# Kernel tuning notes

Measured on AMD Instinct MI355X. Metric: run time of the kernel, lower is better.

The kernel has to match this reference:

```python
import jax, jax.numpy as jnp
import numpy as np

N_HEAD = 8

def setup_inputs() -> dict:
    key = jax.random.key(0)
    ks = jax.random.split(key, 5)
    B, T, C = 2, 4096, 512
    x = jax.random.normal(ks[0], (B, T, C), dtype=jnp.float32)
    w_attn = jax.random.normal(ks[1], (3 * C, C), dtype=jnp.float32) * (1.0 / np.sqrt(C))
    b_attn = jax.random.normal(ks[2], (3 * C,), dtype=jnp.float32) * 0.02
    w_proj = jax.random.normal(ks[3], (C, C), dtype=jnp.float32) * (1.0 / np.sqrt(C))
    b_proj = jax.random.normal(ks[4], (C,), dtype=jnp.float32) * 0.02
    return {"x": x, "w_attn": w_attn, "b_attn": b_attn, "w_proj": w_proj, "b_proj": b_proj}

def reference(x, w_attn, b_attn, w_proj, b_proj):
    B, T, C = x.shape
    H = N_HEAD
    D = C // H  # head dim
    qkv = x @ w_attn.T + b_attn  # [B,T,3C]
    q, k, v = jnp.split(qkv, 3, axis=-1)
    # b t (h d) -> b h t d
    def to_heads(t):
        return t.reshape(B, T, H, D).transpose(0, 2, 1, 3)
    q, k, v = to_heads(q), to_heads(k), to_heads(v)
    scale = 1.0 / np.sqrt(D).astype(np.float32)
    att = jnp.einsum('bhqd,bhkd->bhqk', q, k) * scale  # [B,H,T,T]
    causal = jnp.tril(jnp.ones((T, T), dtype=bool))
    att = jnp.where(causal[None, None], att, jnp.float32(-jnp.inf))
    att = jax.nn.softmax(att, axis=-1)
    y = jnp.einsum('bhqk,bhkd->bhqd', att, v)  # [B,H,T,D]
    y = y.transpose(0, 2, 1, 3).reshape(B, T, C)
    return y @ w_proj.T + b_proj
```

## Files before the change

### kernel.cpp

```cpp
#include <hip/hip_runtime.h>

typedef __attribute__((ext_vector_type(8))) __bf16 bf16x8;
typedef __attribute__((ext_vector_type(4))) __bf16 bf16x4;
typedef __attribute__((ext_vector_type(4))) float f32x4;
typedef __attribute__((ext_vector_type(16))) float f32x16;
typedef __attribute__((ext_vector_type(4))) unsigned uint32x4;
typedef __attribute__((ext_vector_type(2))) unsigned uint32x2;

#define AS1 __attribute__((address_space(1)))
#define AS3 __attribute__((address_space(3)))

#if __has_builtin(__builtin_amdgcn_exp2f)
#define EXP2(x) __builtin_amdgcn_exp2f(x)
#else
#define EXP2(x) exp2f(x)
#endif

#define QSCALE 0.18033688011112042f

#define N_X 4194304
#define N_WA 786432
#define N_WP 262144
__global__ __launch_bounds__(256) void convert_all_k(const float* __restrict__ x,
                                                     const float* __restrict__ wa,
                                                     const float* __restrict__ wp,
                                                     __bf16* __restrict__ xb,
                                                     __bf16* __restrict__ wab,
                                                     __bf16* __restrict__ wpb) {
  int i = (blockIdx.x * 256 + threadIdx.x) * 8;
  const float* src;
  __bf16* dst;
  int off;
  if (i < N_X)              { src = x;  dst = xb;  off = i; }
  else if (i < N_X + N_WA)  { src = wa; dst = wab; off = i - N_X; }
  else if (i < N_X + N_WA + N_WP) { src = wp; dst = wpb; off = i - N_X - N_WA; }
  else return;
  float4 v0 = *reinterpret_cast<const float4*>(src + off);
  float4 v1 = *reinterpret_cast<const float4*>(src + off + 4);
  bf16x8 o;
  o[0] = (__bf16)v0.x; o[1] = (__bf16)v0.y; o[2] = (__bf16)v0.z; o[3] = (__bf16)v0.w;
  o[4] = (__bf16)v1.x; o[5] = (__bf16)v1.y; o[6] = (__bf16)v1.z; o[7] = (__bf16)v1.w;
  *reinterpret_cast<bf16x8*>(dst + off) = o;
}

__global__ __launch_bounds__(256) void gemm_bt(const __bf16* __restrict__ A,
                                               const __bf16* __restrict__ Bm,
                                               const float* __restrict__ bias,
                                               void* __restrict__ outp,
                                               __bf16* __restrict__ vtout,
                                               int M, int N, int K) {
  __shared__ __bf16 smem[24576];
  const int tid = threadIdx.x;
  const int lane = tid & 63;
  const int w = tid >> 6;
  const int wm = w >> 1, wn = w & 1;
  const int ll = lane & 15, lh = lane >> 4;
  const int bid = (int)blockIdx.x;
  const int NT = N >> 7;
  const int xcd = bid & 7, lidx = bid >> 3;
  const int m0 = (xcd * 8 + lidx / NT) * 128;
  const int n0 = (lidx % NT) * 128;
  f32x4 acc[4][4] = {};

  auto stage = [&](int k0, int ss) {
    __bf16* al = smem + ss * 8192;
    __bf16* bl = al + 4096;
#pragma unroll
    for (int i = 0; i < 2; ++i) {
      int ch = i * 256 + tid;
      int r = ch >> 2, cs = (ch & 3) ^ ((r >> 1) & 3);
      const __bf16* ga = A + (size_t)(m0 + r) * K + k0 + cs * 8;
      __builtin_amdgcn_global_load_lds((const AS1 void*)ga, (AS3 void*)(al + ch * 8), 16, 0, 0);
      const __bf16* gb = Bm + (size_t)(n0 + r) * K + k0 + cs * 8;
      __builtin_amdgcn_global_load_lds((const AS1 void*)gb, (AS3 void*)(bl + ch * 8), 16, 0, 0);
    }
  };

  const int nsteps = K >> 5;
  stage(0, 0);
  __builtin_amdgcn_sched_barrier(0);
  stage(32, 1);
  __builtin_amdgcn_sched_barrier(0);
  int slot = 0;
  for (int t = 0; t < nsteps; ++t) {
    if (t + 1 < nsteps) asm volatile("s_waitcnt vmcnt(4)" ::: "memory");
    else                asm volatile("s_waitcnt vmcnt(0)" ::: "memory");
    __builtin_amdgcn_sched_barrier(0);
    __builtin_amdgcn_s_barrier();
    __builtin_amdgcn_sched_barrier(0);
    if (t + 2 < nsteps) {
      int s2 = slot + 2; if (s2 >= 3) s2 -= 3;
      stage((t + 2) << 5, s2);
      __builtin_amdgcn_sched_barrier(0);
    }
    const __bf16* al = smem + slot * 8192;
    const __bf16* bl = al + 4096;
    bf16x8 af[4], bfr[4];
#pragma unroll
    for (int m = 0; m < 4; ++m) {
      int R = wm * 64 + m * 16 + ll;
      af[m] = *reinterpret_cast<const bf16x8*>(al + R * 32 + ((lh ^ ((R >> 1) & 3)) << 3));
    }
#pragma unroll
    for (int n = 0; n < 4; ++n) {
      int R = wn * 64 + n * 16 + ll;
      bfr[n] = *reinterpret_cast<const bf16x8*>(bl + R * 32 + ((lh ^ ((R >> 1) & 3)) << 3));
    }
    __builtin_amdgcn_s_setprio(1);
#pragma unroll
    for (int m = 0; m < 4; ++m)
#pragma unroll
      for (int n = 0; n < 4; ++n)
        acc[m][n] = __builtin_amdgcn_mfma_f32_16x16x32_bf16(af[m], bfr[n], acc[m][n], 0, 0, 0);
    __builtin_amdgcn_s_setprio(0);
    __builtin_amdgcn_sched_barrier(0);
    slot = (slot == 2) ? 0 : slot + 1;
  }
  if (n0 < 1024) {
    __syncthreads();
    __bf16* tb = smem + w * 4096;
    const float sc = (n0 < 512) ? (float)QSCALE : 1.0f;
#pragma unroll
    for (int m = 0; m < 4; ++m)
#pragma unroll
      for (int n = 0; n < 4; ++n) {
        float bs = bias[n0 + wn * 64 + n * 16 + ll];
#pragma unroll
        for (int r = 0; r < 4; ++r)
          tb[(m * 16 + lh * 4 + r) * 64 + n * 16 + ll] = (__bf16)((acc[m][n][r] + bs) * sc);
      }
    const int rsub = lane >> 3, csub = (lane & 7) * 8;
#pragma unroll
    for (int i = 0; i < 8; ++i) {
      bf16x8 vv = *reinterpret_cast<const bf16x8*>(tb + (i * 8 + rsub) * 64 + csub);
      *reinterpret_cast<bf16x8*>((__bf16*)outp +
          (size_t)(m0 + wm * 64 + i * 8 + rsub) * N + n0 + wn * 64 + csub) = vv;
    }
  } else {
    __syncthreads();
    __bf16* tb = smem + w * 4096;
#pragma unroll
    for (int m = 0; m < 4; ++m) {
      const int rb = m * 4 + lh;
#pragma unroll
      for (int n = 0; n < 4; ++n) {
        const int col = n * 16 + ll;
        float bs = bias[n0 + wn * 64 + col];
        bf16x4 pk;
#pragma unroll
        for (int r = 0; r < 4; ++r) pk[r] = (__bf16)(acc[m][n][r] + bs);
        *reinterpret_cast<bf16x4*>(tb + col * 64 + ((rb ^ (col & 15)) << 2)) = pk;
      }
    }
    const int b = m0 >> 12;
    const int tbase = (m0 + wm * 64) & 4095;
    const int dbase = n0 - 1024 + wn * 64;
    const int dl = lane >> 3;
    const int j1 = (lane & 7) * 2;
    const int tloc = (lane & 7) * 8;
#pragma unroll
    for (int i = 0; i < 8; ++i) {
      const int col = i * 8 + dl;
      uint32x2 lo = *reinterpret_cast<const uint32x2*>(tb + col * 64 + ((j1 ^ (col & 15)) << 2));
      uint32x2 hi = *reinterpret_cast<const uint32x2*>(tb + col * 64 + (((j1 + 1) ^ (col & 15)) << 2));
      uint32x4 full = {lo[0], lo[1], hi[0], hi[1]};
      *reinterpret_cast<uint32x4*>(vtout + ((size_t)(b * 512 + dbase + col)) * 4096 + tbase + tloc) = full;
    }
  }
}

__global__ __launch_bounds__(256) void gemm2_k(const __bf16* __restrict__ A,
                                               const __bf16* __restrict__ Bm,
                                               const float* __restrict__ bias,
                                               float* __restrict__ out) {
  __shared__ __bf16 smem[12288];
  const int K = 512, N = 512;
  const int tid = threadIdx.x, lane = tid & 63, w = tid >> 6;
  const int wm = w >> 1, wn = w & 1;
  const int ll = lane & 15, lh = lane >> 4;
  const int bid = (int)blockIdx.x;
  const int xcd = bid & 7, lidx = bid >> 3;
  const int m0 = (xcd * 16 + (lidx >> 3)) * 64;
  const int n0 = (lidx & 7) * 64;
  f32x4 acc[2][2] = {};

  const int r = tid >> 2, cs = (tid & 3) ^ ((r >> 1) & 3);
  const __bf16* ga = A + (size_t)(m0 + r) * K + cs * 8;
  const __bf16* gb = Bm + (size_t)(n0 + r) * K + cs * 8;

  auto stage = [&](int k0, int ss) {
    __bf16* al = smem + ss * 4096;
    __builtin_amdgcn_global_load_lds((const AS1 void*)(ga + k0), (AS3 void*)(al + tid * 8), 16, 0, 0);
    __builtin_amdgcn_global_load_lds((const AS1 void*)(gb + k0), (AS3 void*)(al + 2048 + tid * 8), 16, 0, 0);
  };

  stage(0, 0);
  __builtin_amdgcn_sched_barrier(0);
  stage(32, 1);
  __builtin_amdgcn_sched_barrier(0);
  int slot = 0;
  for (int t = 0; t < 16; ++t) {
    if (t + 1 < 16) asm volatile("s_waitcnt vmcnt(2)" ::: "memory");
    else            asm volatile("s_waitcnt vmcnt(0)" ::: "memory");
    __builtin_amdgcn_sched_barrier(0);
    __builtin_amdgcn_s_barrier();
    __builtin_amdgcn_sched_barrier(0);
    if (t + 2 < 16) {
      int s2 = slot + 2; if (s2 >= 3) s2 -= 3;
      stage((t + 2) << 5, s2);
      __builtin_amdgcn_sched_barrier(0);
    }
    const __bf16* al = smem + slot * 4096;
    const __bf16* bl = al + 2048;
    bf16x8 af[2], bfr[2];
#pragma unroll
    for (int m = 0; m < 2; ++m) {
      int R = wm * 32 + m * 16 + ll;
      af[m] = *reinterpret_cast<const bf16x8*>(al + R * 32 + ((lh ^ ((R >> 1) & 3)) << 3));
    }
#pragma unroll
    for (int n = 0; n < 2; ++n) {
      int R = wn * 32 + n * 16 + ll;
      bfr[n] = *reinterpret_cast<const bf16x8*>(bl + R * 32 + ((lh ^ ((R >> 1) & 3)) << 3));
    }
    __builtin_amdgcn_s_setprio(1);
#pragma unroll
    for (int m = 0; m < 2; ++m)
#pragma unroll
      for (int n = 0; n < 2; ++n)
        acc[m][n] = __builtin_amdgcn_mfma_f32_16x16x32_bf16(af[m], bfr[n], acc[m][n], 0, 0, 0);
    __builtin_amdgcn_s_setprio(0);
    __builtin_amdgcn_sched_barrier(0);
    slot = (slot == 2) ? 0 : slot + 1;
  }
#pragma unroll
  for (int m = 0; m < 2; ++m) {
    int gm = m0 + wm * 32 + m * 16 + lh * 4;
#pragma unroll
    for (int n = 0; n < 2; ++n) {
      int gn = n0 + wn * 32 + n * 16 + ll;
      float bs = bias[gn];
#pragma unroll
      for (int r4 = 0; r4 < 4; ++r4)
        out[(size_t)(gm + r4) * N + gn] = acc[m][n][r4] + bs;
    }
  }
}

struct Tbl { unsigned short t[204]; };
constexpr Tbl build_tbl() {
  Tbl T{};
  int sizes[204] = {};
  int n = 0;
  for (int p = 0; p < 2; ++p)
    for (int qx = 0; qx < 32; ++qx) {
      int total = 2 * qx + 2;
      int nch = (total + 11) / 12;
      int cum = 0;
      for (int q = 0; q < qx; ++q) cum += (2 * q + 13) / 12;
      for (int c = 0; c < nch; ++c) {
        int sz = total - 12 * c; if (sz > 12) sz = 12;
        T.t[n] = (unsigned short)(qx | (c << 5) | (p << 8) | ((cum + c) << 9));
        sizes[n] = sz;
        ++n;
      }
    }
  for (int i = 1; i < n; ++i) {
    unsigned short tv = T.t[i]; int sv = sizes[i];
    int j = i - 1;
    while (j >= 0 && sizes[j] < sv) { T.t[j + 1] = T.t[j]; sizes[j + 1] = sizes[j]; --j; }
    T.t[j + 1] = tv; sizes[j + 1] = sv;
  }
  return T;
}
__device__ __constant__ Tbl g_tbl = build_tbl();

__device__ inline unsigned cvtpk(float lo, float hi_) {
  unsigned r;
  asm("v_cvt_pk_bf16_f32 %0, %1, %2" : "=v"(r) : "v"(lo), "v"(hi_));
  return r;
}

__global__ __launch_bounds__(256, 4) void attn_k(const __bf16* __restrict__ qkv,
                                                 const __bf16* __restrict__ vt,
                                                 __bf16* __restrict__ opart,
                                                 float* __restrict__ lpart,
                                                 __bf16* __restrict__ y) {
  __shared__ __bf16 k_lds[3][64 * 64];
  __shared__ __bf16 v_lds[2][64 * 64];
  const int tid = threadIdx.x, lane = tid & 63, w = tid >> 6;
  const int hi = lane >> 5, q31 = lane & 31;
  const int swz = q31 & 7;

  const int bid = (int)blockIdx.x;
  const int e = g_tbl.t[bid >> 3];
  const int qx = e & 31, c = (e >> 5) & 7, p = (e >> 8) & 1, j = e >> 9;
  const int bh = (bid & 7) * 2 + p;
  const int pslot = bh * 102 + j;
  const int b = bh >> 3, h = bh & 7;
  const int q0 = qx * 128;
  const int qw0 = q0 + w * 32;
  const int t0 = 12 * c;
  const int t1 = min(12 * c + 12, 2 * qx + 2);

  const __bf16* qp = qkv + (size_t)b * 4096 * 1536 + h * 64;
  const __bf16* vtp = vt + (size_t)(b * 512 + h * 64) * 4096;

  const int rr = tid >> 3;
  const int cs = (tid & 7) ^ (rr & 7);
  const __bf16* kg = qp + 512 + (size_t)(t0 * 64 + rr) * 1536 + cs * 8;
  const __bf16* vg = vtp + (size_t)rr * 4096 + t0 * 64 + cs * 8;

  bf16x8 qf[4];
  {
    const __bf16* qr = qp + (size_t)(qw0 + q31) * 1536 + hi * 8;
#pragma unroll
    for (int d = 0; d < 4; ++d) qf[d] = *reinterpret_cast<const bf16x8*>(qr + d * 16);
  }

  f32x16 o0 = {}, o1 = {};
  float l_run = 0.f;

  auto stageK = [&](int ks) {
    __builtin_amdgcn_global_load_lds((const AS1 void*)kg,
        (AS3 void*)(&k_lds[ks][w * 512]), 16, 0, 0);
    __builtin_amdgcn_global_load_lds((const AS1 void*)(kg + 32 * 1536),
        (AS3 void*)(&k_lds[ks][2048 + w * 512]), 16, 0, 0);
    kg += 64 * 1536;
  };
  auto stageV = [&](int vs) {
    __builtin_amdgcn_global_load_lds((const AS1 void*)vg,
        (AS3 void*)(&v_lds[vs][w * 512]), 16, 0, 0);
    __builtin_amdgcn_global_load_lds((const AS1 void*)(vg + 32 * 4096),
        (AS3 void*)(&v_lds[vs][2048 + w * 512]), 16, 0, 0);
    vg += 64;
  };

  stageV(0);
  __builtin_amdgcn_sched_barrier(0);
  stageK(0);
  __builtin_amdgcn_sched_barrier(0);
  stageK(1);
  __builtin_amdgcn_sched_barrier(0);

  int kslot = 0, vslot = 0;
  for (int t = t0; t < t1; ++t) {
    if (t + 1 < t1) asm volatile("s_waitcnt vmcnt(2)" ::: "memory");
    else            asm volatile("s_waitcnt vmcnt(0)" ::: "memory");
    __builtin_amdgcn_sched_barrier(0);
    __builtin_amdgcn_s_barrier();
    __builtin_amdgcn_sched_barrier(0);
    if (t + 1 < t1) {
      stageV(vslot ^ 1);
      __builtin_amdgcn_sched_barrier(0);
      if (t + 2 < t1) {
        int k2 = kslot + 2; if (k2 >= 3) k2 -= 3;
        stageK(k2);
        __builtin_amdgcn_sched_barrier(0);
      }
    }
    const int kv0 = t * 64;
    if (kv0 <= qw0 + 31) {
      f32x16 s0 = {}, s1 = {};
      __builtin_amdgcn_s_setprio(1);
#pragma unroll
      for (int d = 0; d < 4; ++d) {
        int c0 = ((d * 2 + hi) ^ swz) * 8;
        s0 = __builtin_amdgcn_mfma_f32_32x32x16_bf16(
            *reinterpret_cast<const bf16x8*>(&k_lds[kslot][q31 * 64 + c0]), qf[d], s0, 0, 0, 0);
        s1 = __builtin_amdgcn_mfma_f32_32x32x16_bf16(
            *reinterpret_cast<const bf16x8*>(&k_lds[kslot][(32 + q31) * 64 + c0]), qf[d], s1, 0, 0, 0);
      }
      __builtin_amdgcn_s_setprio(0);
      if (kv0 + 63 > qw0) {
        const int q = qw0 + q31;
#pragma unroll
        for (int r = 0; r < 16; ++r) {
          int crow = (r & 3) + 8 * (r >> 2) + 4 * hi;
          if (kv0 + crow > q) s0[r] = -1e30f;
          if (kv0 + 32 + crow > q) s1[r] = -1e30f;
        }
      }
#pragma unroll
      for (int r = 0; r < 16; ++r) s0[r] = EXP2(s0[r]);
#pragma unroll
      for (int r = 0; r < 16; ++r) s1[r] = EXP2(s1[r]);
      {
        float a8[8];
#pragma unroll
        for (int r = 0; r < 8; ++r)
          a8[r] = (s0[r] + s0[r + 8]) + (s1[r] + s1[r + 8]);
        l_run += (((a8[0] + a8[1]) + (a8[2] + a8[3])) + ((a8[4] + a8[5]) + (a8[6] + a8[7])));
      }
      uint32x4 pa[4];
#pragma unroll
      for (int half = 0; half < 2; ++half) {
        const int bse = half * 8;
        {
          unsigned x1 = cvtpk(s0[bse + 0], s0[bse + 1]);
          unsigned y1 = cvtpk(s0[bse + 4], s0[bse + 5]);
          asm("v_permlane32_swap_b32 %0, %1" : "+v"(x1), "+v"(y1));
          pa[half][0] = x1; pa[half][2] = y1;
          unsigned x2 = cvtpk(s0[bse + 2], s0[bse + 3]);
          unsigned y2 = cvtpk(s0[bse + 6], s0[bse + 7]);
          asm("v_permlane32_swap_b32 %0, %1" : "+v"(x2), "+v"(y2));
          pa[half][1] = x2; pa[half][3] = y2;
        }
        {
          unsigned x1 = cvtpk(s1[bse + 0], s1[bse + 1]);
          unsigned y1 = cvtpk(s1[bse + 4], s1[bse + 5]);
          asm("v_permlane32_swap_b32 %0, %1" : "+v"(x1), "+v"(y1));
          pa[2 + half][0] = x1; pa[2 + half][2] = y1;
          unsigned x2 = cvtpk(s1[bse + 2], s1[bse + 3]);
          unsigned y2 = cvtpk(s1[bse + 6], s1[bse + 7]);
          asm("v_permlane32_swap_b32 %0, %1" : "+v"(x2), "+v"(y2));
          pa[2 + half][1] = x2; pa[2 + half][3] = y2;
        }
      }
      __builtin_amdgcn_s_setprio(1);
#pragma unroll
      for (int ks = 0; ks < 4; ++ks) {
        int c0 = ((ks * 2 + hi) ^ swz) * 8;
        bf16x8 pfrag = __builtin_bit_cast(bf16x8, pa[ks]);
        o0 = __builtin_amdgcn_mfma_f32_32x32x16_bf16(
            *reinterpret_cast<const bf16x8*>(&v_lds[vslot][q31 * 64 + c0]), pfrag, o0, 0, 0, 0);
        o1 = __builtin_amdgcn_mfma_f32_32x32x16_bf16(
            *reinterpret_cast<const bf16x8*>(&v_lds[vslot][(32 + q31) * 64 + c0]), pfrag, o1, 0, 0, 0);
      }
      __builtin_amdgcn_s_setprio(0);
    }
    __builtin_amdgcn_sched_barrier(0);
    kslot = (kslot == 2) ? 0 : kslot + 1;
    vslot ^= 1;
  }

  l_run += __shfl_xor(l_run, 32);

  const int rloc = w * 32 + q31;
  if (t0 == 0 && t1 == 2 * qx + 2) {
    const float inv = 1.f / l_run;
    __bf16* yr = y + ((size_t)b * 4096 + qw0 + q31) * 512 + h * 64;
#pragma unroll
    for (int g = 0; g < 4; ++g) {
      bf16x4 v0, v1;
#pragma unroll
      for (int jj = 0; jj < 4; ++jj) {
        v0[jj] = (__bf16)(o0[g * 4 + jj] * inv);
        v1[jj] = (__bf16)(o1[g * 4 + jj] * inv);
      }
      *reinterpret_cast<bf16x4*>(yr + 8 * g + 4 * hi) = v0;
      *reinterpret_cast<bf16x4*>(yr + 32 + 8 * g + 4 * hi) = v1;
    }
  } else {
    __bf16* ob = opart + ((size_t)pslot * 128 + rloc) * 64;
#pragma unroll
    for (int g = 0; g < 4; ++g) {
      bf16x4 v0, v1;
#pragma unroll
      for (int jj = 0; jj < 4; ++jj) {
        v0[jj] = (__bf16)(o0[g * 4 + jj]);
        v1[jj] = (__bf16)(o1[g * 4 + jj]);
      }
      *reinterpret_cast<bf16x4*>(ob + 8 * g + 4 * hi) = v0;
      *reinterpret_cast<bf16x4*>(ob + 32 + 8 * g + 4 * hi) = v1;
    }
    if (hi == 0) lpart[pslot * 128 + rloc] = l_run;
  }
}

__global__ __launch_bounds__(256) void combine_k(const __bf16* __restrict__ opart,
                                                 const float* __restrict__ lpart,
                                                 __bf16* __restrict__ y) {
  const int bid = (int)blockIdx.x;
  const int xcd = bid & 7, idx = bid >> 3;
  const int p = (idx >= 26) ? 1 : 0;
  const int bh = xcd * 2 + p;
  const int qx = 6 + (idx - 26 * p);
  const int b = bh >> 3, h = bh & 7;
  const int n = (2 * qx + 13) / 12;
  int cum = 0;
  for (int q = 0; q < qx; ++q) cum += (2 * q + 13) / 12;
  const int g0 = bh * 102 + cum;
  const int tid = threadIdx.x;
  const int r = tid >> 1, dh = (tid & 1) * 32;

  float W = 0.f;
  float acc[32] = {};
  for (int i = 0; i < n; ++i) {
    W += lpart[(g0 + i) * 128 + r];
    const __bf16* op = opart + ((size_t)(g0 + i) * 128 + r) * 64 + dh;
#pragma unroll
    for (int jj = 0; jj < 4; ++jj) {
      bf16x8 v = *reinterpret_cast<const bf16x8*>(op + jj * 8);
#pragma unroll
      for (int e = 0; e < 8; ++e) acc[jj * 8 + e] += (float)v[e];
    }
  }
  const float inv = 1.f / W;
  __bf16* yr = y + ((size_t)b * 4096 + qx * 128 + r) * 512 + h * 64 + dh;
#pragma unroll
  for (int jj = 0; jj < 4; ++jj) {
    bf16x8 ov;
#pragma unroll
    for (int e = 0; e < 8; ++e) ov[e] = (__bf16)(acc[jj * 8 + e] * inv);
    *reinterpret_cast<bf16x8*>(yr + jj * 8) = ov;
  }
}

extern "C" void kernel_launch(void* const* d_in, const int* in_sizes, int n_in,
                              void* d_out, int out_size, void* d_ws, size_t ws_size,
                              hipStream_t stream) {
  const float* x      = (const float*)d_in[0];
  const float* w_attn = (const float*)d_in[1];
  const float* b_attn = (const float*)d_in[2];
  const float* w_proj = (const float*)d_in[3];
  const float* b_proj = (const float*)d_in[4];
  float* out = (float*)d_out;

  const int Bv = 2, T = 4096, C = 512;
  const int M = Bv * T;

  const size_t NPART = (size_t)1632 * 128 * 64;
  __bf16* opart  = (__bf16*)d_ws;
  __bf16* x_bf   = opart;
  __bf16* wa_bf  = opart + NPART;
  __bf16* wp_bf  = wa_bf + (size_t)786432;
  __bf16* qkv_bf = wp_bf + (size_t)262144;
  __bf16* y_bf   = qkv_bf + (size_t)12582912;
  __bf16* vt_bf  = y_bf + (size_t)4194304;
  float*  lpart  = (float*)(vt_bf + (size_t)4194304);

  const int ntot = N_X + N_WA + N_WP;
  convert_all_k<<<(ntot / 8 + 255) / 256, 256, 0, stream>>>(x, w_attn, w_proj, x_bf, wa_bf, wp_bf);

  gemm_bt<<<dim3((3 * C / 128) * (M / 128)), 256, 0, stream>>>(x_bf, wa_bf, b_attn, qkv_bf, vt_bf, M, 3 * C, C);
  attn_k<<<dim3(1632), 256, 0, stream>>>(qkv_bf, vt_bf, opart, lpart, y_bf);
  combine_k<<<dim3(416), 256, 0, stream>>>(opart, lpart, y_bf);
  gemm2_k<<<dim3(1024), 256, 0, stream>>>(y_bf, wp_bf, b_proj, out);
}
```

Measured before the change: 97.65 us.

## Fuse split-KV combine into attention kernel via last-block atomic counter

Removes the separate combine_k launch. Each attention block that writes a partial output bumps a per-(bh,query-tile) atomic counter, and the last-arriving block sums the partials and writes y. This saves one kernel launch and its tail, and lets the reduction overlap with other attention blocks. In exchange it adds a memset, threadfences and a serial reduction inside one block of the attention grid.

Measured after the change: 224.8 us. +130.2%, slower.

```diff
diff --git a/kernel.cpp b/kernel.cpp
--- a/kernel.cpp
+++ b/kernel.cpp
@@ -285,6 +285,7 @@
                                                  const __bf16* __restrict__ vt,
                                                  __bf16* __restrict__ opart,
                                                  float* __restrict__ lpart,
+                                                 unsigned* __restrict__ counters,
                                                  __bf16* __restrict__ y) {
   __shared__ __bf16 k_lds[3][64 * 64];
   __shared__ __bf16 v_lds[2][64 * 64];
@@ -465,45 +466,41 @@
       *reinterpret_cast<bf16x4*>(ob + 32 + 8 * g + 4 * hi) = v1;
     }
     if (hi == 0) lpart[pslot * 128 + rloc] = l_run;
-  }
-}
-
-__global__ __launch_bounds__(256) void combine_k(const __bf16* __restrict__ opart,
-                                                 const float* __restrict__ lpart,
-                                                 __bf16* __restrict__ y) {
-  const int bid = (int)blockIdx.x;
-  const int xcd = bid & 7, idx = bid >> 3;
-  const int p = (idx >= 26) ? 1 : 0;
-  const int bh = xcd * 2 + p;
-  const int qx = 6 + (idx - 26 * p);
-  const int b = bh >> 3, h = bh & 7;
-  const int n = (2 * qx + 13) / 12;
-  int cum = 0;
-  for (int q = 0; q < qx; ++q) cum += (2 * q + 13) / 12;
-  const int g0 = bh * 102 + cum;
-  const int tid = threadIdx.x;
-  const int r = tid >> 1, dh = (tid & 1) * 32;
-
-  float W = 0.f;
-  float acc[32] = {};
-  for (int i = 0; i < n; ++i) {
-    W += lpart[(g0 + i) * 128 + r];
-    const __bf16* op = opart + ((size_t)(g0 + i) * 128 + r) * 64 + dh;
-#pragma unroll
-    for (int jj = 0; jj < 4; ++jj) {
-      bf16x8 v = *reinterpret_cast<const bf16x8*>(op + jj * 8);
-#pragma unroll
-      for (int e = 0; e < 8; ++e) acc[jj * 8 + e] += (float)v[e];
-    }
-  }
-  const float inv = 1.f / W;
-  __bf16* yr = y + ((size_t)b * 4096 + qx * 128 + r) * 512 + h * 64 + dh;
-#pragma unroll
-  for (int jj = 0; jj < 4; ++jj) {
-    bf16x8 ov;
-#pragma unroll
-    for (int e = 0; e < 8; ++e) ov[e] = (__bf16)(acc[jj * 8 + e] * inv);
-    *reinterpret_cast<bf16x8*>(yr + jj * 8) = ov;
+
+    const int nch = (2 * qx + 13) / 12;
+    const int g0 = pslot - c;
+    __syncthreads();
+    int* flag = (int*)&k_lds[0][0];
+    if (tid == 0) {
+      __threadfence();
+      *flag = (int)atomicAdd(&counters[bh * 26 + (qx - 6)], 1u);
+    }
+    __syncthreads();
+    if (*flag == nch - 1) {
+      __threadfence();
+      const int r = tid >> 1, dh = (tid & 1) * 32;
+      float W = 0.f;
+      float acc[32] = {};
+      for (int i = 0; i < nch; ++i) {
+        W += lpart[(g0 + i) * 128 + r];
+        const __bf16* op = opart + ((size_t)(g0 + i) * 128 + r) * 64 + dh;
+#pragma unroll
+        for (int jj = 0; jj < 4; ++jj) {
+          bf16x8 v = *reinterpret_cast<const bf16x8*>(op + jj * 8);
+#pragma unroll
+          for (int ee = 0; ee < 8; ++ee) acc[jj * 8 + ee] += (float)v[ee];
+        }
+      }
+      const float inv = 1.f / W;
+      __bf16* yr = y + ((size_t)b * 4096 + qx * 128 + r) * 512 + h * 64 + dh;
+#pragma unroll
+      for (int jj = 0; jj < 4; ++jj) {
+        bf16x8 ov;
+#pragma unroll
+        for (int ee = 0; ee < 8; ++ee) ov[ee] = (__bf16)(acc[jj * 8 + ee] * inv);
+        *reinterpret_cast<bf16x8*>(yr + jj * 8) = ov;
+      }
+    }
   }
 }
 
@@ -529,12 +526,14 @@
   __bf16* y_bf   = qkv_bf + (size_t)12582912;
   __bf16* vt_bf  = y_bf + (size_t)4194304;
   float*  lpart  = (float*)(vt_bf + (size_t)4194304);
+  unsigned* counters = (unsigned*)(lpart + 208896);
+
+  hipMemsetAsync(counters, 0, 416 * sizeof(unsigned), stream);
 
   const int ntot = N_X + N_WA + N_WP;
   convert_all_k<<<(ntot / 8 + 255) / 256, 256, 0, stream>>>(x, w_attn, w_proj, x_bf, wa_bf, wp_bf);
 
   gemm_bt<<<dim3((3 * C / 128) * (M / 128)), 256, 0, stream>>>(x_bf, wa_bf, b_attn, qkv_bf, vt_bf, M, 3 * C, C);
-  attn_k<<<dim3(1632), 256, 0, stream>>>(qkv_bf, vt_bf, opart, lpart, y_bf);
-  combine_k<<<dim3(416), 256, 0, stream>>>(opart, lpart, y_bf);
+  attn_k<<<dim3(1632), 256, 0, stream>>>(qkv_bf, vt_bf, opart, lpart, counters, y_bf);
   gemm2_k<<<dim3(1024), 256, 0, stream>>>(y_bf, wp_bf, b_proj, out);
 }
```
